# Optimization experiments

Hardware: AMD Instinct MI355X
Metric: run time of the kernel (lower is better)

The kernel has to match this reference:

```python
import jax, jax.numpy as jnp
import numpy as np

SEQ_LEN, BATCH, INPUT, HID, LAYERS, TARGET_LEN = 120, 2048, 6, 64, 4, 120


def _cell(x_t, h, c, Wih, Whh, b):
    # torch LSTM gate order: input, forget, cell(g), output
    gates = x_t @ Wih.T + h @ Whh.T + b  # [B, 4H]
    i, f, g, o = jnp.split(gates, 4, axis=-1)
    c_new = jax.nn.sigmoid(f) * c + jax.nn.sigmoid(i) * jnp.tanh(g)
    h_new = jax.nn.sigmoid(o) * jnp.tanh(c_new)
    return h_new, c_new


def _stack_step(h, c, x_t, Wih0, Wih, Whh, b):
    # one time step through all stacked layers; h, c: [L, B, H]
    hs, cs = [], []
    inp = x_t
    L = Whh.shape[0]
    for l in range(L):
        W = Wih0 if l == 0 else Wih[l - 1]
        hn, cn = _cell(inp, h[l], c[l], W, Whh[l], b[l])
        hs.append(hn)
        cs.append(cn)
        inp = hn
    return jnp.stack(hs), jnp.stack(cs), inp


def setup_inputs() -> dict:
    key = jax.random.key(0)
    ks = jax.random.split(key, 11)
    s = 1.0 / np.sqrt(HID)  # torch LSTM uniform init scale
    u = lambda k, shp: jax.random.uniform(k, shp, jnp.float32, -s, s)
    return {
        "x": jax.random.normal(ks[0], (SEQ_LEN, BATCH, INPUT), jnp.float32),
        "enc_Wih0": u(ks[1], (4 * HID, INPUT)),
        "enc_Wih": u(ks[2], (LAYERS - 1, 4 * HID, HID)),
        "enc_Whh": u(ks[3], (LAYERS, 4 * HID, HID)),
        "enc_b": u(ks[4], (LAYERS, 4 * HID)),
        "dec_Wih0": u(ks[5], (4 * HID, INPUT)),
        "dec_Wih": u(ks[6], (LAYERS - 1, 4 * HID, HID)),
        "dec_Whh": u(ks[7], (LAYERS, 4 * HID, HID)),
        "dec_b": u(ks[8], (LAYERS, 4 * HID)),
        "lin_W": u(ks[9], (INPUT, HID)),
        "lin_b": u(ks[10], (INPUT,)),
        "target_len": TARGET_LEN,
    }


def reference(x, enc_Wih0, enc_Wih, enc_Whh, enc_b,
              dec_Wih0, dec_Wih, dec_Whh, dec_b, lin_W, lin_b, target_len):
    L, B, H = enc_Whh.shape[0], x.shape[1], enc_Whh.shape[-1]
    h0 = jnp.zeros((L, B, H), x.dtype)

    # ---- encoder: stacked LSTM over the input sequence (zero init state) ----
    def enc_step(carry, x_t):
        h, c = carry
        h, c, _ = _stack_step(h, c, x_t, enc_Wih0, enc_Wih, enc_Whh, enc_b)
        return (h, c), None

    (h, c), _ = jax.lax.scan(enc_step, (h0, h0), x)

    # ---- decoder: recursive one-step decode for target_len steps ----
    def dec_step(carry, _):
        h, c, inp = carry
        h, c, top = _stack_step(h, c, inp, dec_Wih0, dec_Wih, dec_Whh, dec_b)
        out = top @ lin_W.T + lin_b  # [B, INPUT]
        return (h, c, out), out

    last_in = x[-1]  # decoder seeded with last observed frame
    _, outputs = jax.lax.scan(dec_step, (h, c, last_in), None, length=target_len)
    return outputs  # [target_len, B, INPUT]
```

## Files before the change

kernel.cpp:

```cpp
#include <hip/hip_runtime.h>


#define S_LEN 120
#define BATCH 2048
#define NIN   6
#define H     64
#define NL    4
#define TLEN  120

#define HPAD 72

#define FRAGS_HALF 60
#define PACK_H8    (2 * FRAGS_HALF * 4 * 64)
#define PROJ_H8    (2 * 64)
#define NPACK      ((PACK_H8 + PROJ_H8) * 8)
#define EPACK_EL   (256 * 64 * 8)
#define NTOT       (NPACK + EPACK_EL)

#define WS_HOFF (768 * 1024)
#define WS_COFF (WS_HOFF + 1024 * 1024)

#define PERM(kk) ((((kk) & 3) << 4) | ((kk) >> 2))
#define PI(c)    ((((c) & 15) << 2) | ((c) >> 4))

typedef _Float16 h8    __attribute__((ext_vector_type(8)));
typedef _Float16 hh2   __attribute__((ext_vector_type(2)));
typedef float    f32x4 __attribute__((ext_vector_type(4)));

__device__ __forceinline__ void bar_lgkm() {
  asm volatile("s_waitcnt lgkmcnt(0)\n\ts_barrier" ::: "memory");
}

__device__ __forceinline__ float swz16(float v) {
  int i = __builtin_bit_cast(int, v);
  i = __builtin_amdgcn_ds_swizzle(i, 0x401F);
  return __builtin_bit_cast(float, i);
}

__global__ void prep_weights(const float* __restrict__ eWih0,
                             const float* __restrict__ eWih,
                             const float* __restrict__ eWhh,
                             const float* __restrict__ dWih0,
                             const float* __restrict__ dWih,
                             const float* __restrict__ dWhh,
                             const float* __restrict__ linW,
                             _Float16* __restrict__ wq) {
  int idx = blockIdx.x * blockDim.x + threadIdx.x;
  if (idx >= NTOT) return;

  if (idx >= NPACK) {
    int p    = idx - NPACK;
    int j    = p & 7;
    int lane = (p >> 3) & 63;
    int fe   = p >> 9;
    int kt   = fe & 3, nt = (fe >> 2) & 15, l = fe >> 6;
    int g    = nt * 16 + (lane & 15);
    int koff = ((lane >> 4) << 3) + j;
    float v = 0.0f;
    if (l == 0) {
      if (kt == 0)      v = (koff < NIN) ? eWih0[g * NIN + koff] : 0.0f;
      else if (kt == 1) v = 0.0f;
      else { int kk = (kt - 2) * 32 + koff; v = eWhh[g * H + PERM(kk)]; }
    } else {
      if (kt < 2) { int kk = kt * 32 + koff;
                    v = eWih[((l - 1) * 256 + g) * H + PERM(kk)]; }
      else        { int kk = (kt - 2) * 32 + koff;
                    v = eWhh[(l * 256 + g) * H + PERM(kk)]; }
    }
    wq[idx] = (_Float16)v;
    return;
  }

  if (idx >= PACK_H8 * 8) {
    int p    = idx - PACK_H8 * 8;
    int j    = p & 7;
    int lane = (p >> 3) & 63;
    int fr   = p >> 9;
    int m    = lane & 15;
    int k    = fr * 32 + ((lane >> 4) << 3) + j;
    wq[idx] = (_Float16)((m < NIN) ? linW[m * H + k] : 0.0f);
    return;
  }

  const int j    = idx & 7;
  const int lane = (idx >> 3) & 63;
  const int wv   = (idx >> 9) & 3;
  const int fh   = idx >> 11;
  const int f    = fh % FRAGS_HALF;
  const int half = fh / FRAGS_HALF;
  const float* Wi0 = half ? dWih0 : eWih0;
  const float* Wi  = half ? dWih  : eWih;
  const float* Wh  = half ? dWhh  : eWhh;
  int l, q, kt;
  if (f < 12) { l = 0; q = f / 3; kt = f % 3; }
  else        { int ff = f - 12; l = 1 + ff / 16; ff %= 16; q = ff / 4; kt = ff % 4; }
  const int g    = q * 64 + wv * 16 + (lane & 15);
  const int k_in = ((lane >> 4) << 3) + j;
  float v;
  if (l == 0) {
    if (kt == 0) v = (k_in < NIN) ? Wi0[g * NIN + k_in] : 0.0f;
    else         v = Wh[g * H + (kt - 1) * 32 + k_in];
  } else {
    if (kt < 2) v = Wi[((l - 1) * 256 + g) * H + kt * 32 + k_in];
    else        v = Wh[(l * 256 + g) * H + (kt - 2) * 32 + k_in];
  }
  wq[idx] = (_Float16)v;
}

__device__ __forceinline__ float rcpf(float x) { return __builtin_amdgcn_rcpf(x); }
__device__ __forceinline__ f32x4 mf(h8 a, h8 b, f32x4 c) {
  return __builtin_amdgcn_mfma_f32_16x16x32_f16(a, b, c, 0, 0, 0);
}
#define SPLAT(v) ((f32x4){(v), (v), (v), (v)})

__device__ __forceinline__ float ew_one(float gi, float gf, float gg, float go,
                                        float& c) {
  gg = fminf(fmaxf(gg, -20.0f), 20.0f);
  float eni = __expf(-gi);
  float e2g = __expf(2.0f * gg);
  float enf = __expf(-gf);
  float eno = __expf(-go);
  c = c * rcpf(1.0f + enf) + (e2g - 1.0f) * rcpf((1.0f + eni) * (e2g + 1.0f));
  float cc = fminf(fmaxf(c, -20.0f), 20.0f);
  float e2c = __expf(2.0f * cc);
  return (e2c - 1.0f) * rcpf((1.0f + eno) * (e2c + 1.0f));
}

__device__ __forceinline__ void cell_ew(f32x4 g0, f32x4 g1, f32x4 g2, f32x4 g3,
                                        f32x4& c, _Float16* outbuf,
                                        int quad, int r16, int sl) {
  #pragma unroll
  for (int r = 0; r < 4; r++) {
    float cv = c[r];
    float hv = ew_one(g0[r], g1[r], g2[r], g3[r], cv);
    c[r] = cv;
    outbuf[(quad * 4 + r) * HPAD + sl * 16 + r16] = (_Float16)hv;
  }
}

__device__ __forceinline__ void precc(const h8 (&w)[8], h8 ar0, h8 ar1,
                                      f32x4 b, f32x4 (&ac)[4]) {
  #pragma unroll
  for (int q = 0; q < 4; q++)
    ac[q] = mf(ar1, w[q * 2 + 1], mf(ar0, w[q * 2], SPLAT(b[q])));
}
__device__ __forceinline__ void fireHc(const h8 (&w)[8], h8 ai0, h8 ai1,
                                       const f32x4 (&ac)[4], f32x4& c,
                                       _Float16* outbuf, int quad, int r16, int sl) {
  f32x4 g0 = mf(ai1, w[1], mf(ai0, w[0], ac[0]));
  f32x4 g1 = mf(ai1, w[3], mf(ai0, w[2], ac[1]));
  f32x4 g2 = mf(ai1, w[5], mf(ai0, w[4], ac[2]));
  f32x4 g3 = mf(ai1, w[7], mf(ai0, w[6], ac[3]));
  cell_ew(g0, g1, g2, g3, c, outbuf, quad, r16, sl);
}
__device__ __forceinline__ void fire0c(const h8 (&w)[4], h8 ax,
                                       const f32x4 (&ac)[4], f32x4& c,
                                       _Float16* outbuf, int quad, int r16, int sl) {
  f32x4 g0 = mf(ax, w[0], ac[0]);
  f32x4 g1 = mf(ax, w[1], ac[1]);
  f32x4 g2 = mf(ax, w[2], ac[2]);
  f32x4 g3 = mf(ax, w[3], ac[3]);
  cell_ew(g0, g1, g2, g3, c, outbuf, quad, r16, sl);
}
__device__ __forceinline__ void readA(const _Float16* buf, int r16, int quad,
                                      h8& a0, h8& a1) {
  a0 = *(const h8*)(buf + r16 * HPAD + quad * 8);
  a1 = *(const h8*)(buf + r16 * HPAD + 32 + quad * 8);
}

__global__ void __launch_bounds__(512, 2)
lstm_enc(const float* __restrict__ X,
         const float* __restrict__ encb,
         const h8* __restrict__ WQ,
         _Float16* __restrict__ hG,
         float* __restrict__ cG) {
  __shared__ _Float16 Hb[NL][2][16][HPAD];
  __shared__ _Float16 Xb[2][16][HPAD];

  const int tid  = threadIdx.x;
  const int wv   = tid >> 6;
  const int lane = tid & 63;
  const int quad = lane >> 4;
  const int r16  = lane & 15;
  const int grp  = wv >> 2;
  const int lw   = wv & 3;
  const int bbase = blockIdx.x * 16;

  {
    float* p = (float*)&Hb[0][0][0][0];
    for (int i = tid; i < 4608; i += 512) p[i] = 0.0f;
    float* px = (float*)&Xb[0][0][0];
    for (int i = tid; i < 1152; i += 512) px[i] = 0.0f;
  }
  if (tid < 16 * NIN) {
    int m = tid / NIN, ii = tid - m * NIN;
    Xb[0][m][ii] = (_Float16)X[((size_t)0 * BATCH + bbase + m) * NIN + ii];
  }

  h8 we[8][4];
  #pragma unroll
  for (int q = 0; q < 4; q++)
    #pragma unroll
    for (int cc = 0; cc < 2; cc++)
      #pragma unroll
      for (int kt = 0; kt < 4; kt++)
        we[q * 2 + cc][kt] =
            WQ[(PACK_H8 + PROJ_H8) +
               ((lw * 64 + (q * 4 + 2 * grp + cc) * 4 + kt) * 64 + lane)];
  float ben[8];
  #pragma unroll
  for (int q = 0; q < 4; q++)
    #pragma unroll
    for (int cc = 0; cc < 2; cc++)
      ben[q * 2 + cc] = encb[lw * 256 + q * 64 + (2 * grp + cc) * 16 + r16];

  f32x4 ce[2];
  ce[0] = SPLAT(0.f); ce[1] = SPLAT(0.f);

  const bool pfLane = (wv == 0) && (lane < 48);
  const int  pe0 = lane * 2, pe1 = pe0 + 1;
  const int  pm0 = pe0 / NIN, pc0 = pe0 % NIN;
  const int  pm1 = pe1 / NIN, pc1 = pe1 % NIN;
  float pf0 = 0.f, pf1 = 0.f;
  if (pfLane) {
    const float* xs = X + ((size_t)1 * BATCH + bbase) * NIN;
    pf0 = xs[pe0]; pf1 = xs[pe1];
  }

  __syncthreads();

  #pragma unroll 1
  for (int i = 0; i < S_LEN + NL - 1; i++) {
    const int p = i & 1;
    const bool active = (i >= lw) && (i - lw < S_LEN);
    if (active) {
      const _Float16* inb = (lw == 0) ? &Xb[p][0][0] : &Hb[lw - 1][p ^ 1][0][0];
      const _Float16* rcb = &Hb[lw][p ^ 1][0][0];
      h8 ai0 = *(const h8*)(inb + r16 * HPAD + quad * 8);
      h8 ai1 = {};
      if (lw) ai1 = *(const h8*)(inb + r16 * HPAD + 32 + quad * 8);
      h8 ar0 = *(const h8*)(rcb + r16 * HPAD + quad * 8);
      h8 ar1 = *(const h8*)(rcb + r16 * HPAD + 32 + quad * 8);

      float nf0 = 0.f, nf1 = 0.f;
      if (pfLane && (i + 2 < S_LEN)) {
        const float* xs = X + ((size_t)(i + 2) * BATCH + bbase) * NIN;
        nf0 = xs[pe0]; nf1 = xs[pe1];
      }

      f32x4 a[8];
      #pragma unroll
      for (int j = 0; j < 8; j++) {
        f32x4 t = SPLAT(ben[j]);
        t = mf(ai0, we[j][0], t);
        if (lw) t = mf(ai1, we[j][1], t);
        t = mf(ar0, we[j][2], t);
        t = mf(ar1, we[j][3], t);
        a[j] = t;
      }

      _Float16* wb = &Hb[lw][p][0][0];
      #pragma unroll
      for (int r = 0; r < 4; r++) {
        hh2 hv;
        #pragma unroll
        for (int cc = 0; cc < 2; cc++) {
          float cv = ce[cc][r];
          hv[cc] = (_Float16)ew_one(a[cc][r], a[2 + cc][r],
                                    a[4 + cc][r], a[6 + cc][r], cv);
          ce[cc][r] = cv;
        }
        *(hh2*)(wb + (quad * 4 + r) * HPAD + 4 * r16 + 2 * grp) = hv;
      }

      if (pfLane && (i + 1 < S_LEN)) {
        Xb[p ^ 1][pm0][pc0] = (_Float16)pf0;
        Xb[p ^ 1][pm1][pc1] = (_Float16)pf1;
      }
      pf0 = nf0; pf1 = nf1;
    }
    bar_lgkm();
  }

  #pragma unroll
  for (int cc = 0; cc < 2; cc++)
    #pragma unroll
    for (int r = 0; r < 4; r++)
      cG[((size_t)lw * BATCH + bbase + quad * 4 + r) * H +
         (2 * grp + cc) * 16 + r16] = ce[cc][r];

  #pragma unroll
  for (int u = 0; u < 8; u++) {
    int i2 = tid + u * 512;
    int c = i2 & 63, m = (i2 >> 6) & 15, l = (i2 >> 10) & 3;
    hG[((size_t)l * BATCH + bbase + m) * H + c] =
        Hb[l][(l + 1) & 1][m][PI(c)];
  }
}

__global__ void __launch_bounds__(512, 2)
lstm_dec(const float* __restrict__ X,
         const float* __restrict__ decb,
         const float* __restrict__ linb,
         const h8* __restrict__ WQ,
         const _Float16* __restrict__ hG,
         const float* __restrict__ cG,
         float* __restrict__ out) {
  __shared__ _Float16 Hb[NL][2][16][HPAD];
  __shared__ f32x4 ACs[NL][4][4][64];

  const int tid   = threadIdx.x;
  const int wv    = tid >> 6;
  const int sl    = wv & 3;
  const int roleP = wv >> 2;
  const int lane  = tid & 63;
  const int quad  = lane >> 4;
  const int r16   = lane & 15;
  const int bbase = blockIdx.x * 16;

  #pragma unroll
  for (int u = 0; u < 8; u++) {
    int i2 = tid + u * 512;
    int l = i2 >> 10, m = (i2 >> 6) & 15, c = i2 & 63;
    Hb[l][1][m][c] = hG[((size_t)l * BATCH + bbase + m) * H + c];
  }
  __syncthreads();

  if (roleP) {
    h8 wp0[8], wpH[3][8];
    #pragma unroll
    for (int e = 0; e < 8; e++) {
      int q = e >> 1, k = e & 1;
      wp0[e] = WQ[((FRAGS_HALF + q * 3 + 1 + k) * 4 + sl) * 64 + lane];
    }
    #pragma unroll
    for (int l = 0; l < 3; l++)
      #pragma unroll
      for (int e = 0; e < 8; e++) {
        int q = e >> 1, k = e & 1;
        wpH[l][e] = WQ[((FRAGS_HALF + 12 + l * 16 + q * 4 + 2 + k) * 4 + sl) * 64 + lane];
      }
    f32x4 b0, b1, b2, b3;
    #pragma unroll
    for (int q = 0; q < 4; q++) {
      b0[q] = decb[0 * 256 + q * 64 + sl * 16 + r16];
      b1[q] = decb[1 * 256 + q * 64 + sl * 16 + r16];
      b2[q] = decb[2 * 256 + q * 64 + sl * 16 + r16];
      b3[q] = decb[3 * 256 + q * 64 + sl * 16 + r16];
    }

    {
      h8 s0, s1;
      f32x4 a[4];
      readA(&Hb[0][1][0][0], r16, quad, s0, s1);
      precc(wp0, s0, s1, b0, a);
      #pragma unroll
      for (int j = 0; j < 4; j++) ACs[0][sl][j][lane] = a[j];
      readA(&Hb[1][1][0][0], r16, quad, s0, s1);
      precc(wpH[0], s0, s1, b1, a);
      #pragma unroll
      for (int j = 0; j < 4; j++) ACs[1][sl][j][lane] = a[j];
      readA(&Hb[2][1][0][0], r16, quad, s0, s1);
      precc(wpH[1], s0, s1, b2, a);
      #pragma unroll
      for (int j = 0; j < 4; j++) ACs[2][sl][j][lane] = a[j];
    }
    bar_lgkm();

    #pragma unroll 1
    for (int t = 0; t < TLEN; t++) {
      const int cur = t & 1, prv = cur ^ 1;
      {
        h8 a0, a1; readA(&Hb[3][prv][0][0], r16, quad, a0, a1);
        f32x4 a[4]; precc(wpH[2], a0, a1, b3, a);
        #pragma unroll
        for (int j = 0; j < 4; j++) ACs[3][sl][j][lane] = a[j];
        bar_lgkm();
      }
      {
        h8 a0, a1; readA(&Hb[0][cur][0][0], r16, quad, a0, a1);
        f32x4 a[4]; precc(wp0, a0, a1, b0, a);
        #pragma unroll
        for (int j = 0; j < 4; j++) ACs[0][sl][j][lane] = a[j];
        bar_lgkm();
      }
      {
        h8 a0, a1; readA(&Hb[1][cur][0][0], r16, quad, a0, a1);
        f32x4 a[4]; precc(wpH[0], a0, a1, b1, a);
        #pragma unroll
        for (int j = 0; j < 4; j++) ACs[1][sl][j][lane] = a[j];
        bar_lgkm();
      }
      {
        h8 a0, a1; readA(&Hb[2][cur][0][0], r16, quad, a0, a1);
        f32x4 a[4]; precc(wpH[1], a0, a1, b2, a);
        #pragma unroll
        for (int j = 0; j < 4; j++) ACs[2][sl][j][lane] = a[j];
        bar_lgkm();
      }
    }
  } else {
    h8 wf0[4], wfH[3][8];
    #pragma unroll
    for (int q = 0; q < 4; q++)
      wf0[q] = WQ[((FRAGS_HALF + q * 3) * 4 + sl) * 64 + lane];
    #pragma unroll
    for (int l = 0; l < 3; l++)
      #pragma unroll
      for (int e = 0; e < 8; e++) {
        int q = e >> 1, k = e & 1;
        wfH[l][e] = WQ[((FRAGS_HALF + 12 + l * 16 + q * 4 + k) * 4 + sl) * 64 + lane];
      }

    f32x4 cs0, cs1, cs2, cs3;
    #pragma unroll
    for (int r = 0; r < 4; r++) {
      cs0[r] = cG[((size_t)0 * BATCH + bbase + quad * 4 + r) * H + sl * 16 + r16];
      cs1[r] = cG[((size_t)1 * BATCH + bbase + quad * 4 + r) * H + sl * 16 + r16];
      cs2[r] = cG[((size_t)2 * BATCH + bbase + quad * 4 + r) * H + sl * 16 + r16];
      cs3[r] = cG[((size_t)3 * BATCH + bbase + quad * 4 + r) * H + sl * 16 + r16];
    }

    h8 lwA0 = WQ[PACK_H8 + lane];
    h8 lwA1 = WQ[PACK_H8 + 64 + lane];
    f32x4 lbq;
    #pragma unroll
    for (int r = 0; r < 4; r++)
      lbq[r] = (quad * 4 + r < NIN) ? linb[quad * 4 + r] : 0.0f;

    h8 xseed = {};
    if (quad == 0) {
      const float* xs = X + ((size_t)(S_LEN - 1) * BATCH + bbase + r16) * NIN;
      #pragma unroll
      for (int j = 0; j < 6; j++) xseed[j] = (_Float16)xs[j];
    }

    bar_lgkm();

    __builtin_amdgcn_s_setprio(1);

    #pragma unroll 1
    for (int t = 0; t < TLEN; t++) {
      const int cur = t & 1, prv = cur ^ 1;
      {
        h8 ar0, ar1;
        readA(&Hb[3][prv][0][0], r16, quad, ar0, ar1);
        h8 ax;
        if (t == 0) {
          ax = xseed;
        } else {
          f32x4 ap = lbq;
          ap = mf(lwA0, ar0, ap);
          ap = mf(lwA1, ar1, ap);
          if (sl == 0) {
            #pragma unroll
            for (int r = 0; r < 4; r++) {
              const int fm = quad * 4 + r;
              if (fm < NIN)
                out[((size_t)(t - 1) * BATCH + bbase + r16) * NIN + fm] = ap[r];
            }
          }
          float x4 = swz16(ap[0]);
          float x5 = swz16(ap[1]);
          h8 xa = {};
          xa[0] = (_Float16)ap[0]; xa[1] = (_Float16)ap[1];
          xa[2] = (_Float16)ap[2]; xa[3] = (_Float16)ap[3];
          xa[4] = (_Float16)x4;    xa[5] = (_Float16)x5;
          h8 zz = {};
          ax = (quad == 0) ? xa : zz;
        }
        f32x4 ac[4];
        #pragma unroll
        for (int j = 0; j < 4; j++) ac[j] = ACs[0][sl][j][lane];
        fire0c(wf0, ax, ac, cs0, &Hb[0][cur][0][0], quad, r16, sl);
        bar_lgkm();
      }
      {
        h8 ai0, ai1;
        readA(&Hb[0][cur][0][0], r16, quad, ai0, ai1);
        f32x4 ac[4];
        #pragma unroll
        for (int j = 0; j < 4; j++) ac[j] = ACs[1][sl][j][lane];
        fireHc(wfH[0], ai0, ai1, ac, cs1, &Hb[1][cur][0][0], quad, r16, sl);
        bar_lgkm();
      }
      {
        h8 ai0, ai1;
        readA(&Hb[1][cur][0][0], r16, quad, ai0, ai1);
        f32x4 ac[4];
        #pragma unroll
        for (int j = 0; j < 4; j++) ac[j] = ACs[2][sl][j][lane];
        fireHc(wfH[1], ai0, ai1, ac, cs2, &Hb[2][cur][0][0], quad, r16, sl);
        bar_lgkm();
      }
      {
        h8 ai0, ai1;
        readA(&Hb[2][cur][0][0], r16, quad, ai0, ai1);
        f32x4 ac[4];
        #pragma unroll
        for (int j = 0; j < 4; j++) ac[j] = ACs[3][sl][j][lane];
        fireHc(wfH[2], ai0, ai1, ac, cs3, &Hb[3][cur][0][0], quad, r16, sl);
        bar_lgkm();
      }
    }

    __builtin_amdgcn_s_setprio(0);

    if (sl == 0) {
      h8 ar0, ar1;
      readA(&Hb[3][1][0][0], r16, quad, ar0, ar1);
      f32x4 ap = lbq;
      ap = mf(lwA0, ar0, ap);
      ap = mf(lwA1, ar1, ap);
      #pragma unroll
      for (int r = 0; r < 4; r++) {
        const int fm = quad * 4 + r;
        if (fm < NIN)
          out[((size_t)(TLEN - 1) * BATCH + bbase + r16) * NIN + fm] = ap[r];
      }
    }
  }
}

extern "C" void kernel_launch(void* const* d_in, const int* in_sizes, int n_in,
                              void* d_out, int out_size, void* d_ws, size_t ws_size,
                              hipStream_t stream) {
  const float* X     = (const float*)d_in[0];
  const float* eWih0 = (const float*)d_in[1];
  const float* eWih  = (const float*)d_in[2];
  const float* eWhh  = (const float*)d_in[3];
  const float* eb    = (const float*)d_in[4];
  const float* dWih0 = (const float*)d_in[5];
  const float* dWih  = (const float*)d_in[6];
  const float* dWhh  = (const float*)d_in[7];
  const float* db    = (const float*)d_in[8];
  const float* lW    = (const float*)d_in[9];
  const float* lb    = (const float*)d_in[10];

  _Float16* wq = (_Float16*)d_ws;
  _Float16* hG = (_Float16*)((char*)d_ws + WS_HOFF);
  float*    cG = (float*)((char*)d_ws + WS_COFF);

  prep_weights<<<(NTOT + 255) / 256, 256, 0, stream>>>(
      eWih0, eWih, eWhh, dWih0, dWih, dWhh, lW, wq);

  lstm_enc<<<BATCH / 16, 512, 0, stream>>>(
      X, eb, (const h8*)wq, hG, cG);

  lstm_dec<<<BATCH / 16, 512, 0, stream>>>(
      X, db, lb, (const h8*)wq, hG, cG, (float*)d_out);
}
```

Before: 531.8 us.

## Split decoder LSTM cell elementwise work between fire and precompute wave groups

In the decoder, the critical-path waves used to compute all four rows of the gate nonlinearities after the MFMA. Now they write half of the gate results (rows 2-3) to shared memory, and the precompute waves pick those up and run the elementwise cell update for those rows. Each wave group keeps half of the cell state. The goal is to shorten the serial elementwise tail on the recurrent critical path. The cost is an extra barrier per layer step and extra LDS traffic. The s_setprio priority boost on the fire waves is also removed.

```diff
diff --git a/kernel.cpp b/kernel.cpp
--- a/kernel.cpp
+++ b/kernel.cpp
@@ -26,6 +26,7 @@
 typedef _Float16 h8    __attribute__((ext_vector_type(8)));
 typedef _Float16 hh2   __attribute__((ext_vector_type(2)));
 typedef float    f32x4 __attribute__((ext_vector_type(4)));
+typedef float    f32x2 __attribute__((ext_vector_type(2)));
 
 __device__ __forceinline__ void bar_lgkm() {
   asm volatile("s_waitcnt lgkmcnt(0)\n\ts_barrier" ::: "memory");
@@ -138,29 +139,25 @@
   }
 }
 
+__device__ __forceinline__ void ew_pair(float g0a, float g0b, float g1a, float g1b,
+                                        float g2a, float g2b, float g3a, float g3b,
+                                        f32x2& c, _Float16* outbuf,
+                                        int quad, int r16, int sl, int rbase) {
+  float cv0 = c[0];
+  float h0 = ew_one(g0a, g1a, g2a, g3a, cv0);
+  c[0] = cv0;
+  outbuf[(quad * 4 + rbase) * HPAD + sl * 16 + r16] = (_Float16)h0;
+  float cv1 = c[1];
+  float h1 = ew_one(g0b, g1b, g2b, g3b, cv1);
+  c[1] = cv1;
+  outbuf[(quad * 4 + rbase + 1) * HPAD + sl * 16 + r16] = (_Float16)h1;
+}
+
 __device__ __forceinline__ void precc(const h8 (&w)[8], h8 ar0, h8 ar1,
                                       f32x4 b, f32x4 (&ac)[4]) {
   #pragma unroll
   for (int q = 0; q < 4; q++)
     ac[q] = mf(ar1, w[q * 2 + 1], mf(ar0, w[q * 2], SPLAT(b[q])));
-}
-__device__ __forceinline__ void fireHc(const h8 (&w)[8], h8 ai0, h8 ai1,
-                                       const f32x4 (&ac)[4], f32x4& c,
-                                       _Float16* outbuf, int quad, int r16, int sl) {
-  f32x4 g0 = mf(ai1, w[1], mf(ai0, w[0], ac[0]));
-  f32x4 g1 = mf(ai1, w[3], mf(ai0, w[2], ac[1]));
-  f32x4 g2 = mf(ai1, w[5], mf(ai0, w[4], ac[2]));
-  f32x4 g3 = mf(ai1, w[7], mf(ai0, w[6], ac[3]));
-  cell_ew(g0, g1, g2, g3, c, outbuf, quad, r16, sl);
-}
-__device__ __forceinline__ void fire0c(const h8 (&w)[4], h8 ax,
-                                       const f32x4 (&ac)[4], f32x4& c,
-                                       _Float16* outbuf, int quad, int r16, int sl) {
-  f32x4 g0 = mf(ax, w[0], ac[0]);
-  f32x4 g1 = mf(ax, w[1], ac[1]);
-  f32x4 g2 = mf(ax, w[2], ac[2]);
-  f32x4 g3 = mf(ax, w[3], ac[3]);
-  cell_ew(g0, g1, g2, g3, c, outbuf, quad, r16, sl);
 }
 __device__ __forceinline__ void readA(const _Float16* buf, int r16, int quad,
                                       h8& a0, h8& a1) {
@@ -308,6 +305,7 @@
          float* __restrict__ out) {
   __shared__ _Float16 Hb[NL][2][16][HPAD];
   __shared__ f32x4 ACs[NL][4][4][64];
+  __shared__ f32x2 GBs[4][4][64];
 
   const int tid   = threadIdx.x;
   const int wv    = tid >> 6;
@@ -348,6 +346,14 @@
       b2[q] = decb[2 * 256 + q * 64 + sl * 16 + r16];
       b3[q] = decb[3 * 256 + q * 64 + sl * 16 + r16];
     }
+    f32x2 cp0, cp1, cp2, cp3;
+    #pragma unroll
+    for (int j = 0; j < 2; j++) {
+      cp0[j] = cG[((size_t)0 * BATCH + bbase + quad * 4 + 2 + j) * H + sl * 16 + r16];
+      cp1[j] = cG[((size_t)1 * BATCH + bbase + quad * 4 + 2 + j) * H + sl * 16 + r16];
+      cp2[j] = cG[((size_t)2 * BATCH + bbase + quad * 4 + 2 + j) * H + sl * 16 + r16];
+      cp3[j] = cG[((size_t)3 * BATCH + bbase + quad * 4 + 2 + j) * H + sl * 16 + r16];
+    }
 
     {
       h8 s0, s1;
@@ -376,6 +382,11 @@
         #pragma unroll
         for (int j = 0; j < 4; j++) ACs[3][sl][j][lane] = a[j];
         bar_lgkm();
+        f32x2 q0 = GBs[sl][0][lane], q1 = GBs[sl][1][lane];
+        f32x2 q2 = GBs[sl][2][lane], q3 = GBs[sl][3][lane];
+        ew_pair(q0[0], q0[1], q1[0], q1[1], q2[0], q2[1], q3[0], q3[1],
+                cp0, &Hb[0][cur][0][0], quad, r16, sl, 2);
+        bar_lgkm();
       }
       {
         h8 a0, a1; readA(&Hb[0][cur][0][0], r16, quad, a0, a1);
@@ -383,6 +394,11 @@
         #pragma unroll
         for (int j = 0; j < 4; j++) ACs[0][sl][j][lane] = a[j];
         bar_lgkm();
+        f32x2 q0 = GBs[sl][0][lane], q1 = GBs[sl][1][lane];
+        f32x2 q2 = GBs[sl][2][lane], q3 = GBs[sl][3][lane];
+        ew_pair(q0[0], q0[1], q1[0], q1[1], q2[0], q2[1], q3[0], q3[1],
+                cp1, &Hb[1][cur][0][0], quad, r16, sl, 2);
+        bar_lgkm();
       }
       {
         h8 a0, a1; readA(&Hb[1][cur][0][0], r16, quad, a0, a1);
@@ -390,6 +406,11 @@
         #pragma unroll
         for (int j = 0; j < 4; j++) ACs[1][sl][j][lane] = a[j];
         bar_lgkm();
+        f32x2 q0 = GBs[sl][0][lane], q1 = GBs[sl][1][lane];
+        f32x2 q2 = GBs[sl][2][lane], q3 = GBs[sl][3][lane];
+        ew_pair(q0[0], q0[1], q1[0], q1[1], q2[0], q2[1], q3[0], q3[1],
+                cp2, &Hb[2][cur][0][0], quad, r16, sl, 2);
+        bar_lgkm();
       }
       {
         h8 a0, a1; readA(&Hb[2][cur][0][0], r16, quad, a0, a1);
@@ -397,6 +418,11 @@
         #pragma unroll
         for (int j = 0; j < 4; j++) ACs[2][sl][j][lane] = a[j];
         bar_lgkm();
+        f32x2 q0 = GBs[sl][0][lane], q1 = GBs[sl][1][lane];
+        f32x2 q2 = GBs[sl][2][lane], q3 = GBs[sl][3][lane];
+        ew_pair(q0[0], q0[1], q1[0], q1[1], q2[0], q2[1], q3[0], q3[1],
+                cp3, &Hb[3][cur][0][0], quad, r16, sl, 2);
+        bar_lgkm();
       }
     }
   } else {
@@ -412,13 +438,13 @@
         wfH[l][e] = WQ[((FRAGS_HALF + 12 + l * 16 + q * 4 + k) * 4 + sl) * 64 + lane];
       }
 
-    f32x4 cs0, cs1, cs2, cs3;
-    #pragma unroll
-    for (int r = 0; r < 4; r++) {
-      cs0[r] = cG[((size_t)0 * BATCH + bbase + quad * 4 + r) * H + sl * 16 + r16];
-      cs1[r] = cG[((size_t)1 * BATCH + bbase + quad * 4 + r) * H + sl * 16 + r16];
-      cs2[r] = cG[((size_t)2 * BATCH + bbase + quad * 4 + r) * H + sl * 16 + r16];
-      cs3[r] = cG[((size_t)3 * BATCH + bbase + quad * 4 + r) * H + sl * 16 + r16];
+    f32x2 cf0, cf1, cf2, cf3;
+    #pragma unroll
+    for (int j = 0; j < 2; j++) {
+      cf0[j] = cG[((size_t)0 * BATCH + bbase + quad * 4 + j) * H + sl * 16 + r16];
+      cf1[j] = cG[((size_t)1 * BATCH + bbase + quad * 4 + j) * H + sl * 16 + r16];
+      cf2[j] = cG[((size_t)2 * BATCH + bbase + quad * 4 + j) * H + sl * 16 + r16];
+      cf3[j] = cG[((size_t)3 * BATCH + bbase + quad * 4 + j) * H + sl * 16 + r16];
     }
 
     h8 lwA0 = WQ[PACK_H8 + lane];
@@ -436,8 +462,6 @@
     }
 
     bar_lgkm();
-
-    __builtin_amdgcn_s_setprio(1);
 
     #pragma unroll 1
     for (int t = 0; t < TLEN; t++) {
@@ -469,42 +493,68 @@
           h8 zz = {};
           ax = (quad == 0) ? xa : zz;
         }
-        f32x4 ac[4];
-        #pragma unroll
-        for (int j = 0; j < 4; j++) ac[j] = ACs[0][sl][j][lane];
-        fire0c(wf0, ax, ac, cs0, &Hb[0][cur][0][0], quad, r16, sl);
+        f32x4 g0 = mf(ax, wf0[0], ACs[0][sl][0][lane]);
+        f32x4 g1 = mf(ax, wf0[1], ACs[0][sl][1][lane]);
+        f32x4 g2 = mf(ax, wf0[2], ACs[0][sl][2][lane]);
+        f32x4 g3 = mf(ax, wf0[3], ACs[0][sl][3][lane]);
+        GBs[sl][0][lane] = (f32x2){g0[2], g0[3]};
+        GBs[sl][1][lane] = (f32x2){g1[2], g1[3]};
+        GBs[sl][2][lane] = (f32x2){g2[2], g2[3]};
+        GBs[sl][3][lane] = (f32x2){g3[2], g3[3]};
+        bar_lgkm();
+        ew_pair(g0[0], g0[1], g1[0], g1[1], g2[0], g2[1], g3[0], g3[1],
+                cf0, &Hb[0][cur][0][0], quad, r16, sl, 0);
         bar_lgkm();
       }
       {
         h8 ai0, ai1;
         readA(&Hb[0][cur][0][0], r16, quad, ai0, ai1);
-        f32x4 ac[4];
-        #pragma unroll
-        for (int j = 0; j < 4; j++) ac[j] = ACs[1][sl][j][lane];
-        fireHc(wfH[0], ai0, ai1, ac, cs1, &Hb[1][cur][0][0], quad, r16, sl);
+        f32x4 g0 = mf(ai1, wfH[0][1], mf(ai0, wfH[0][0], ACs[1][sl][0][lane]));
+        f32x4 g1 = mf(ai1, wfH[0][3], mf(ai0, wfH[0][2], ACs[1][sl][1][lane]));
+        f32x4 g2 = mf(ai1, wfH[0][5], mf(ai0, wfH[0][4], ACs[1][sl][2][lane]));
+        f32x4 g3 = mf(ai1, wfH[0][7], mf(ai0, wfH[0][6], ACs[1][sl][3][lane]));
+        GBs[sl][0][lane] = (f32x2){g0[2], g0[3]};
+        GBs[sl][1][lane] = (f32x2){g1[2], g1[3]};
+        GBs[sl][2][lane] = (f32x2){g2[2], g2[3]};
+        GBs[sl][3][lane] = (f32x2){g3[2], g3[3]};
+        bar_lgkm();
+        ew_pair(g0[0], g0[1], g1[0], g1[1], g2[0], g2[1], g3[0], g3[1],
+                cf1, &Hb[1][cur][0][0], quad, r16, sl, 0);
         bar_lgkm();
       }
       {
         h8 ai0, ai1;
         readA(&Hb[1][cur][0][0], r16, quad, ai0, ai1);
-        f32x4 ac[4];
-        #pragma unroll
-        for (int j = 0; j < 4; j++) ac[j] = ACs[2][sl][j][lane];
-        fireHc(wfH[1], ai0, ai1, ac, cs2, &Hb[2][cur][0][0], quad, r16, sl);
+        f32x4 g0 = mf(ai1, wfH[1][1], mf(ai0, wfH[1][0], ACs[2][sl][0][lane]));
+        f32x4 g1 = mf(ai1, wfH[1][3], mf(ai0, wfH[1][2], ACs[2][sl][1][lane]));
+        f32x4 g2 = mf(ai1, wfH[1][5], mf(ai0, wfH[1][4], ACs[2][sl][2][lane]));
+        f32x4 g3 = mf(ai1, wfH[1][7], mf(ai0, wfH[1][6], ACs[2][sl][3][lane]));
+        GBs[sl][0][lane] = (f32x2){g0[2], g0[3]};
+        GBs[sl][1][lane] = (f32x2){g1[2], g1[3]};
+        GBs[sl][2][lane] = (f32x2){g2[2], g2[3]};
+        GBs[sl][3][lane] = (f32x2){g3[2], g3[3]};
+        bar_lgkm();
+        ew_pair(g0[0], g0[1], g1[0], g1[1], g2[0], g2[1], g3[0], g3[1],
+                cf2, &Hb[2][cur][0][0], quad, r16, sl, 0);
         bar_lgkm();
       }
       {
         h8 ai0, ai1;
         readA(&Hb[2][cur][0][0], r16, quad, ai0, ai1);
-        f32x4 ac[4];
-        #pragma unroll
-        for (int j = 0; j < 4; j++) ac[j] = ACs[3][sl][j][lane];
-        fireHc(wfH[2], ai0, ai1, ac, cs3, &Hb[3][cur][0][0], quad, r16, sl);
-        bar_lgkm();
-      }
-    }
-
-    __builtin_amdgcn_s_setprio(0);
+        f32x4 g0 = mf(ai1, wfH[2][1], mf(ai0, wfH[2][0], ACs[3][sl][0][lane]));
+        f32x4 g1 = mf(ai1, wfH[2][3], mf(ai0, wfH[2][2], ACs[3][sl][1][lane]));
+        f32x4 g2 = mf(ai1, wfH[2][5], mf(ai0, wfH[2][4], ACs[3][sl][2][lane]));
+        f32x4 g3 = mf(ai1, wfH[2][7], mf(ai0, wfH[2][6], ACs[3][sl][3][lane]));
+        GBs[sl][0][lane] = (f32x2){g0[2], g0[3]};
+        GBs[sl][1][lane] = (f32x2){g1[2], g1[3]};
+        GBs[sl][2][lane] = (f32x2){g2[2], g2[3]};
+        GBs[sl][3][lane] = (f32x2){g3[2], g3[3]};
+        bar_lgkm();
+        ew_pair(g0[0], g0[1], g1[0], g1[1], g2[0], g2[1], g3[0], g3[1],
+                cf3, &Hb[3][cur][0][0], quad, r16, sl, 0);
+        bar_lgkm();
+      }
+    }
 
     if (sl == 0) {
       h8 ar0, ar1;
```

Result: slower. 605.6 us (+13.9%).

## Split decoder cell elementwise work across producer and consumer waves

Applied to the files above, without the earlier changes.

The decoder is restructured so all eight waves run one lockstep time loop. Producer waves still precompute the recurrent (h·Whh + b) partials, but now they also run the input-gate MFMAs and handle half of the batch rows' elementwise cell updates; consumer waves handle the other half. The goal is to halve the serial transcendental and elementwise latency on each layer's critical path. In exchange, the gate MFMAs are computed redundantly by both roles, each wave holds more weight registers, and the s_setprio priority hint is dropped.

```diff
diff --git a/kernel.cpp b/kernel.cpp
--- a/kernel.cpp
+++ b/kernel.cpp
@@ -26,6 +26,7 @@
 typedef _Float16 h8    __attribute__((ext_vector_type(8)));
 typedef _Float16 hh2   __attribute__((ext_vector_type(2)));
 typedef float    f32x4 __attribute__((ext_vector_type(4)));
+typedef float    f32x2 __attribute__((ext_vector_type(2)));
 
 __device__ __forceinline__ void bar_lgkm() {
   asm volatile("s_waitcnt lgkmcnt(0)\n\ts_barrier" ::: "memory");
@@ -126,16 +127,18 @@
   return (e2c - 1.0f) * rcpf((1.0f + eno) * (e2c + 1.0f));
 }
 
-__device__ __forceinline__ void cell_ew(f32x4 g0, f32x4 g1, f32x4 g2, f32x4 g3,
-                                        f32x4& c, _Float16* outbuf,
-                                        int quad, int r16, int sl) {
-  #pragma unroll
-  for (int r = 0; r < 4; r++) {
-    float cv = c[r];
-    float hv = ew_one(g0[r], g1[r], g2[r], g3[r], cv);
-    c[r] = cv;
-    outbuf[(quad * 4 + r) * HPAD + sl * 16 + r16] = (_Float16)hv;
-  }
+__device__ __forceinline__ void ew_pair(const f32x4& g0, const f32x4& g1,
+                                        const f32x4& g2, const f32x4& g3,
+                                        f32x2& c, _Float16* outbuf,
+                                        int quad, int r16, int sl, int rb) {
+  float cv0 = c[0];
+  float h0 = ew_one(g0[rb], g1[rb], g2[rb], g3[rb], cv0);
+  c[0] = cv0;
+  outbuf[(quad * 4 + rb) * HPAD + sl * 16 + r16] = (_Float16)h0;
+  float cv1 = c[1];
+  float h1 = ew_one(g0[rb + 1], g1[rb + 1], g2[rb + 1], g3[rb + 1], cv1);
+  c[1] = cv1;
+  outbuf[(quad * 4 + rb + 1) * HPAD + sl * 16 + r16] = (_Float16)h1;
 }
 
 __device__ __forceinline__ void precc(const h8 (&w)[8], h8 ar0, h8 ar1,
@@ -143,24 +146,6 @@
   #pragma unroll
   for (int q = 0; q < 4; q++)
     ac[q] = mf(ar1, w[q * 2 + 1], mf(ar0, w[q * 2], SPLAT(b[q])));
-}
-__device__ __forceinline__ void fireHc(const h8 (&w)[8], h8 ai0, h8 ai1,
-                                       const f32x4 (&ac)[4], f32x4& c,
-                                       _Float16* outbuf, int quad, int r16, int sl) {
-  f32x4 g0 = mf(ai1, w[1], mf(ai0, w[0], ac[0]));
-  f32x4 g1 = mf(ai1, w[3], mf(ai0, w[2], ac[1]));
-  f32x4 g2 = mf(ai1, w[5], mf(ai0, w[4], ac[2]));
-  f32x4 g3 = mf(ai1, w[7], mf(ai0, w[6], ac[3]));
-  cell_ew(g0, g1, g2, g3, c, outbuf, quad, r16, sl);
-}
-__device__ __forceinline__ void fire0c(const h8 (&w)[4], h8 ax,
-                                       const f32x4 (&ac)[4], f32x4& c,
-                                       _Float16* outbuf, int quad, int r16, int sl) {
-  f32x4 g0 = mf(ax, w[0], ac[0]);
-  f32x4 g1 = mf(ax, w[1], ac[1]);
-  f32x4 g2 = mf(ax, w[2], ac[2]);
-  f32x4 g3 = mf(ax, w[3], ac[3]);
-  cell_ew(g0, g1, g2, g3, c, outbuf, quad, r16, sl);
 }
 __device__ __forceinline__ void readA(const _Float16* buf, int r16, int quad,
                                       h8& a0, h8& a1) {
@@ -317,6 +302,7 @@
   const int quad  = lane >> 4;
   const int r16   = lane & 15;
   const int bbase = blockIdx.x * 16;
+  const int rb    = roleP ? 2 : 0;
 
   #pragma unroll
   for (int u = 0; u < 8; u++) {
@@ -326,8 +312,44 @@
   }
   __syncthreads();
 
+  h8 wf0[4], wfH[3][8];
+  #pragma unroll
+  for (int q = 0; q < 4; q++)
+    wf0[q] = WQ[((FRAGS_HALF + q * 3) * 4 + sl) * 64 + lane];
+  #pragma unroll
+  for (int l = 0; l < 3; l++)
+    #pragma unroll
+    for (int e = 0; e < 8; e++) {
+      int q = e >> 1, k = e & 1;
+      wfH[l][e] = WQ[((FRAGS_HALF + 12 + l * 16 + q * 4 + k) * 4 + sl) * 64 + lane];
+    }
+
+  h8 lwA0 = WQ[PACK_H8 + lane];
+  h8 lwA1 = WQ[PACK_H8 + 64 + lane];
+  f32x4 lbq;
+  #pragma unroll
+  for (int r = 0; r < 4; r++)
+    lbq[r] = (quad * 4 + r < NIN) ? linb[quad * 4 + r] : 0.0f;
+
+  h8 xseed = {};
+  if (quad == 0) {
+    const float* xs = X + ((size_t)(S_LEN - 1) * BATCH + bbase + r16) * NIN;
+    #pragma unroll
+    for (int j = 0; j < 6; j++) xseed[j] = (_Float16)xs[j];
+  }
+
+  f32x2 c0, c1, c2, c3;
+  #pragma unroll
+  for (int j = 0; j < 2; j++) {
+    c0[j] = cG[((size_t)0 * BATCH + bbase + quad * 4 + rb + j) * H + sl * 16 + r16];
+    c1[j] = cG[((size_t)1 * BATCH + bbase + quad * 4 + rb + j) * H + sl * 16 + r16];
+    c2[j] = cG[((size_t)2 * BATCH + bbase + quad * 4 + rb + j) * H + sl * 16 + r16];
+    c3[j] = cG[((size_t)3 * BATCH + bbase + quad * 4 + rb + j) * H + sl * 16 + r16];
+  }
+
+  h8 wp0[8], wpH[3][8];
+  f32x4 b0, b1, b2, b3;
   if (roleP) {
-    h8 wp0[8], wpH[3][8];
     #pragma unroll
     for (int e = 0; e < 8; e++) {
       int q = e >> 1, k = e & 1;
@@ -340,7 +362,6 @@
         int q = e >> 1, k = e & 1;
         wpH[l][e] = WQ[((FRAGS_HALF + 12 + l * 16 + q * 4 + 2 + k) * 4 + sl) * 64 + lane];
       }
-    f32x4 b0, b1, b2, b3;
     #pragma unroll
     for (int q = 0; q < 4; q++) {
       b0[q] = decb[0 * 256 + q * 64 + sl * 16 + r16];
@@ -348,176 +369,124 @@
       b2[q] = decb[2 * 256 + q * 64 + sl * 16 + r16];
       b3[q] = decb[3 * 256 + q * 64 + sl * 16 + r16];
     }
-
+    h8 s0, s1;
+    f32x4 a[4];
+    readA(&Hb[0][1][0][0], r16, quad, s0, s1);
+    precc(wp0, s0, s1, b0, a);
+    #pragma unroll
+    for (int j = 0; j < 4; j++) ACs[0][sl][j][lane] = a[j];
+    readA(&Hb[1][1][0][0], r16, quad, s0, s1);
+    precc(wpH[0], s0, s1, b1, a);
+    #pragma unroll
+    for (int j = 0; j < 4; j++) ACs[1][sl][j][lane] = a[j];
+    readA(&Hb[2][1][0][0], r16, quad, s0, s1);
+    precc(wpH[1], s0, s1, b2, a);
+    #pragma unroll
+    for (int j = 0; j < 4; j++) ACs[2][sl][j][lane] = a[j];
+  }
+
+  bar_lgkm();
+
+  #pragma unroll 1
+  for (int t = 0; t < TLEN; t++) {
+    const int cur = t & 1, prv = cur ^ 1;
     {
-      h8 s0, s1;
-      f32x4 a[4];
-      readA(&Hb[0][1][0][0], r16, quad, s0, s1);
-      precc(wp0, s0, s1, b0, a);
-      #pragma unroll
-      for (int j = 0; j < 4; j++) ACs[0][sl][j][lane] = a[j];
-      readA(&Hb[1][1][0][0], r16, quad, s0, s1);
-      precc(wpH[0], s0, s1, b1, a);
-      #pragma unroll
-      for (int j = 0; j < 4; j++) ACs[1][sl][j][lane] = a[j];
-      readA(&Hb[2][1][0][0], r16, quad, s0, s1);
-      precc(wpH[1], s0, s1, b2, a);
-      #pragma unroll
-      for (int j = 0; j < 4; j++) ACs[2][sl][j][lane] = a[j];
-    }
-    bar_lgkm();
-
-    #pragma unroll 1
-    for (int t = 0; t < TLEN; t++) {
-      const int cur = t & 1, prv = cur ^ 1;
-      {
-        h8 a0, a1; readA(&Hb[3][prv][0][0], r16, quad, a0, a1);
-        f32x4 a[4]; precc(wpH[2], a0, a1, b3, a);
+      h8 ar0, ar1;
+      readA(&Hb[3][prv][0][0], r16, quad, ar0, ar1);
+      if (roleP) {
+        f32x4 a[4]; precc(wpH[2], ar0, ar1, b3, a);
         #pragma unroll
         for (int j = 0; j < 4; j++) ACs[3][sl][j][lane] = a[j];
-        bar_lgkm();
-      }
-      {
-        h8 a0, a1; readA(&Hb[0][cur][0][0], r16, quad, a0, a1);
-        f32x4 a[4]; precc(wp0, a0, a1, b0, a);
+      }
+      h8 ax;
+      if (t == 0) {
+        ax = xseed;
+      } else {
+        f32x4 ap = lbq;
+        ap = mf(lwA0, ar0, ap);
+        ap = mf(lwA1, ar1, ap);
+        if (!roleP && sl == 0) {
+          #pragma unroll
+          for (int r = 0; r < 4; r++) {
+            const int fm = quad * 4 + r;
+            if (fm < NIN)
+              out[((size_t)(t - 1) * BATCH + bbase + r16) * NIN + fm] = ap[r];
+          }
+        }
+        float x4 = swz16(ap[0]);
+        float x5 = swz16(ap[1]);
+        h8 xa = {};
+        xa[0] = (_Float16)ap[0]; xa[1] = (_Float16)ap[1];
+        xa[2] = (_Float16)ap[2]; xa[3] = (_Float16)ap[3];
+        xa[4] = (_Float16)x4;    xa[5] = (_Float16)x5;
+        h8 zz = {};
+        ax = (quad == 0) ? xa : zz;
+      }
+      f32x4 g0 = mf(ax, wf0[0], ACs[0][sl][0][lane]);
+      f32x4 g1 = mf(ax, wf0[1], ACs[0][sl][1][lane]);
+      f32x4 g2 = mf(ax, wf0[2], ACs[0][sl][2][lane]);
+      f32x4 g3 = mf(ax, wf0[3], ACs[0][sl][3][lane]);
+      ew_pair(g0, g1, g2, g3, c0, &Hb[0][cur][0][0], quad, r16, sl, rb);
+      bar_lgkm();
+    }
+    {
+      h8 ai0, ai1;
+      readA(&Hb[0][cur][0][0], r16, quad, ai0, ai1);
+      if (roleP) {
+        f32x4 a[4]; precc(wp0, ai0, ai1, b0, a);
         #pragma unroll
         for (int j = 0; j < 4; j++) ACs[0][sl][j][lane] = a[j];
-        bar_lgkm();
-      }
-      {
-        h8 a0, a1; readA(&Hb[1][cur][0][0], r16, quad, a0, a1);
-        f32x4 a[4]; precc(wpH[0], a0, a1, b1, a);
+      }
+      f32x4 g0 = mf(ai1, wfH[0][1], mf(ai0, wfH[0][0], ACs[1][sl][0][lane]));
+      f32x4 g1 = mf(ai1, wfH[0][3], mf(ai0, wfH[0][2], ACs[1][sl][1][lane]));
+      f32x4 g2 = mf(ai1, wfH[0][5], mf(ai0, wfH[0][4], ACs[1][sl][2][lane]));
+      f32x4 g3 = mf(ai1, wfH[0][7], mf(ai0, wfH[0][6], ACs[1][sl][3][lane]));
+      ew_pair(g0, g1, g2, g3, c1, &Hb[1][cur][0][0], quad, r16, sl, rb);
+      bar_lgkm();
+    }
+    {
+      h8 ai0, ai1;
+      readA(&Hb[1][cur][0][0], r16, quad, ai0, ai1);
+      if (roleP) {
+        f32x4 a[4]; precc(wpH[0], ai0, ai1, b1, a);
         #pragma unroll
         for (int j = 0; j < 4; j++) ACs[1][sl][j][lane] = a[j];
-        bar_lgkm();
-      }
-      {
-        h8 a0, a1; readA(&Hb[2][cur][0][0], r16, quad, a0, a1);
-        f32x4 a[4]; precc(wpH[1], a0, a1, b2, a);
+      }
+      f32x4 g0 = mf(ai1, wfH[1][1], mf(ai0, wfH[1][0], ACs[2][sl][0][lane]));
+      f32x4 g1 = mf(ai1, wfH[1][3], mf(ai0, wfH[1][2], ACs[2][sl][1][lane]));
+      f32x4 g2 = mf(ai1, wfH[1][5], mf(ai0, wfH[1][4], ACs[2][sl][2][lane]));
+      f32x4 g3 = mf(ai1, wfH[1][7], mf(ai0, wfH[1][6], ACs[2][sl][3][lane]));
+      ew_pair(g0, g1, g2, g3, c2, &Hb[2][cur][0][0], quad, r16, sl, rb);
+      bar_lgkm();
+    }
+    {
+      h8 ai0, ai1;
+      readA(&Hb[2][cur][0][0], r16, quad, ai0, ai1);
+      if (roleP) {
+        f32x4 a[4]; precc(wpH[1], ai0, ai1, b2, a);
         #pragma unroll
         for (int j = 0; j < 4; j++) ACs[2][sl][j][lane] = a[j];
-        bar_lgkm();
-      }
-    }
-  } else {
-    h8 wf0[4], wfH[3][8];
-    #pragma unroll
-    for (int q = 0; q < 4; q++)
-      wf0[q] = WQ[((FRAGS_HALF + q * 3) * 4 + sl) * 64 + lane];
-    #pragma unroll
-    for (int l = 0; l < 3; l++)
-      #pragma unroll
-      for (int e = 0; e < 8; e++) {
-        int q = e >> 1, k = e & 1;
-        wfH[l][e] = WQ[((FRAGS_HALF + 12 + l * 16 + q * 4 + k) * 4 + sl) * 64 + lane];
-      }
-
-    f32x4 cs0, cs1, cs2, cs3;
+      }
+      f32x4 g0 = mf(ai1, wfH[2][1], mf(ai0, wfH[2][0], ACs[3][sl][0][lane]));
+      f32x4 g1 = mf(ai1, wfH[2][3], mf(ai0, wfH[2][2], ACs[3][sl][1][lane]));
+      f32x4 g2 = mf(ai1, wfH[2][5], mf(ai0, wfH[2][4], ACs[3][sl][2][lane]));
+      f32x4 g3 = mf(ai1, wfH[2][7], mf(ai0, wfH[2][6], ACs[3][sl][3][lane]));
+      ew_pair(g0, g1, g2, g3, c3, &Hb[3][cur][0][0], quad, r16, sl, rb);
+      bar_lgkm();
+    }
+  }
+
+  if (!roleP && sl == 0) {
+    h8 ar0, ar1;
+    readA(&Hb[3][1][0][0], r16, quad, ar0, ar1);
+    f32x4 ap = lbq;
+    ap = mf(lwA0, ar0, ap);
+    ap = mf(lwA1, ar1, ap);
     #pragma unroll
     for (int r = 0; r < 4; r++) {
-      cs0[r] = cG[((size_t)0 * BATCH + bbase + quad * 4 + r) * H + sl * 16 + r16];
-      cs1[r] = cG[((size_t)1 * BATCH + bbase + quad * 4 + r) * H + sl * 16 + r16];
-      cs2[r] = cG[((size_t)2 * BATCH + bbase + quad * 4 + r) * H + sl * 16 + r16];
-      cs3[r] = cG[((size_t)3 * BATCH + bbase + quad * 4 + r) * H + sl * 16 + r16];
-    }
-
-    h8 lwA0 = WQ[PACK_H8 + lane];
-    h8 lwA1 = WQ[PACK_H8 + 64 + lane];
-    f32x4 lbq;
-    #pragma unroll
-    for (int r = 0; r < 4; r++)
-      lbq[r] = (quad * 4 + r < NIN) ? linb[quad * 4 + r] : 0.0f;
-
-    h8 xseed = {};
-    if (quad == 0) {
-      const float* xs = X + ((size_t)(S_LEN - 1) * BATCH + bbase + r16) * NIN;
-      #pragma unroll
-      for (int j = 0; j < 6; j++) xseed[j] = (_Float16)xs[j];
-    }
-
-    bar_lgkm();
-
-    __builtin_amdgcn_s_setprio(1);
-
-    #pragma unroll 1
-    for (int t = 0; t < TLEN; t++) {
-      const int cur = t & 1, prv = cur ^ 1;
-      {
-        h8 ar0, ar1;
-        readA(&Hb[3][prv][0][0], r16, quad, ar0, ar1);
-        h8 ax;
-        if (t == 0) {
-          ax = xseed;
-        } else {
-          f32x4 ap = lbq;
-          ap = mf(lwA0, ar0, ap);
-          ap = mf(lwA1, ar1, ap);
-          if (sl == 0) {
-            #pragma unroll
-            for (int r = 0; r < 4; r++) {
-              const int fm = quad * 4 + r;
-              if (fm < NIN)
-                out[((size_t)(t - 1) * BATCH + bbase + r16) * NIN + fm] = ap[r];
-            }
-          }
-          float x4 = swz16(ap[0]);
-          float x5 = swz16(ap[1]);
-          h8 xa = {};
-          xa[0] = (_Float16)ap[0]; xa[1] = (_Float16)ap[1];
-          xa[2] = (_Float16)ap[2]; xa[3] = (_Float16)ap[3];
-          xa[4] = (_Float16)x4;    xa[5] = (_Float16)x5;
-          h8 zz = {};
-          ax = (quad == 0) ? xa : zz;
-        }
-        f32x4 ac[4];
-        #pragma unroll
-        for (int j = 0; j < 4; j++) ac[j] = ACs[0][sl][j][lane];
-        fire0c(wf0, ax, ac, cs0, &Hb[0][cur][0][0], quad, r16, sl);
-        bar_lgkm();
-      }
-      {
-        h8 ai0, ai1;
-        readA(&Hb[0][cur][0][0], r16, quad, ai0, ai1);
-        f32x4 ac[4];
-        #pragma unroll
-        for (int j = 0; j < 4; j++) ac[j] = ACs[1][sl][j][lane];
-        fireHc(wfH[0], ai0, ai1, ac, cs1, &Hb[1][cur][0][0], quad, r16, sl);
-        bar_lgkm();
-      }
-      {
-        h8 ai0, ai1;
-        readA(&Hb[1][cur][0][0], r16, quad, ai0, ai1);
-        f32x4 ac[4];
-        #pragma unroll
-        for (int j = 0; j < 4; j++) ac[j] = ACs[2][sl][j][lane];
-        fireHc(wfH[1], ai0, ai1, ac, cs2, &Hb[2][cur][0][0], quad, r16, sl);
-        bar_lgkm();
-      }
-      {
-        h8 ai0, ai1;
-        readA(&Hb[2][cur][0][0], r16, quad, ai0, ai1);
-        f32x4 ac[4];
-        #pragma unroll
-        for (int j = 0; j < 4; j++) ac[j] = ACs[3][sl][j][lane];
-        fireHc(wfH[2], ai0, ai1, ac, cs3, &Hb[3][cur][0][0], quad, r16, sl);
-        bar_lgkm();
-      }
-    }
-
-    __builtin_amdgcn_s_setprio(0);
-
-    if (sl == 0) {
-      h8 ar0, ar1;
-      readA(&Hb[3][1][0][0], r16, quad, ar0, ar1);
-      f32x4 ap = lbq;
-      ap = mf(lwA0, ar0, ap);
-      ap = mf(lwA1, ar1, ap);
-      #pragma unroll
-      for (int r = 0; r < 4; r++) {
-        const int fm = quad * 4 + r;
-        if (fm < NIN)
-          out[((size_t)(TLEN - 1) * BATCH + bbase + r16) * NIN + fm] = ap[r];
-      }
+      const int fm = quad * 4 + r;
+      if (fm < NIN)
+        out[((size_t)(TLEN - 1) * BATCH + bbase + r16) * NIN + fm] = ap[r];
     }
   }
 }
```

After: 982.0 us. +84.7%, slower.
